# Optimization experiments

Hardware: AMD Instinct MI355X
Metric: run time of the kernel (lower is better)

Reference implementation:

```python
import jax, jax.numpy as jnp
import numpy as np

V, C, T = 4096, 32, 512


def setup_inputs() -> dict:
    key = jax.random.key(0)
    ks = jax.random.split(key, 6)
    return {
        "x": jax.random.normal(ks[0], (V, C, T), dtype=jnp.float32),
        "U_1": jax.random.normal(ks[1], (V,), dtype=jnp.float32),
        "U_2": jax.random.normal(ks[2], (C, V), dtype=jnp.float32),
        "U_3": jax.random.normal(ks[3], (C,), dtype=jnp.float32),
        "b_e": jax.random.normal(ks[4], (C, T, T), dtype=jnp.float32),
        "V_e": jax.random.normal(ks[5], (T, T), dtype=jnp.float32),
    }


def reference(x, U_1, U_2, U_3, b_e, V_e):
    # x: (V, C, T)
    # lhs = (x.permute(2,1,0) @ U_1) @ U_2  -> (T, C) @ (C, V) = (T, V)
    tmp = jnp.einsum("vct,v->tc", x, U_1)          # (T, C)
    lhs = tmp @ U_2                                   # (T, V)
    # rhs = x.permute(2,0,1) @ U_3 -> (T, V)
    rhs = jnp.einsum("vct,c->tv", x, U_3)           # (T, V)
    product = rhs @ lhs.T                             # (T, T)
    # sigmoid(product + b_e) broadcasts to (C, T, T); V_e @ ... -> (C, T, T)
    E = jnp.einsum("ts,csr->ctr", V_e, jax.nn.sigmoid(product + b_e))
    # max-subtract / exp / sum over dim 1 == softmax over axis 1
    return jax.nn.softmax(E, axis=1)
```

## Files before the change

### kernel.cpp

```cpp
#include <hip/hip_runtime.h>

#define V_N 4096
#define C_N 32
#define T_N 512

typedef float f32x4 __attribute__((ext_vector_type(4)));
typedef __bf16 bf16x8 __attribute__((ext_vector_type(8)));

__device__ inline f32x4 fma4(f32x4 a, float b, f32x4 c) {
    f32x4 r;
    r.x = fmaf(a.x, b, c.x); r.y = fmaf(a.y, b, c.y);
    r.z = fmaf(a.z, b, c.z); r.w = fmaf(a.w, b, c.w);
    return r;
}

__global__ __launch_bounds__(256, 1) void k_rt(const float* __restrict__ x,
                                               const float* __restrict__ U1,
                                               const float* __restrict__ U2,
                                               const float* __restrict__ U3,
                                               float* __restrict__ partT,
                                               float* __restrict__ partG) {
    const int vc = blockIdx.x >> 1;
    const int half = blockIdx.x & 1;
    const int tid = threadIdx.x;
    const int w = tid >> 6;
    const int l = tid & 63;
    const int v0 = vc * 16;

    __shared__ f32x4 lsum[2][4][64];

    float u3loc[8];
#pragma unroll
    for (int i = 0; i < 8; ++i) u3loc[i] = U3[w * 8 + i];

    f32x4 accT[8], gacc[8];
#pragma unroll
    for (int i = 0; i < 8; ++i) { accT[i] = (f32x4)0.f; gacc[i] = (f32x4)0.f; }

    const float* xbase = x + (size_t)v0 * (C_N * T_N) + half * 256 + l * 4;

#pragma unroll 1
    for (int vi = 0; vi < 16; ++vi) {
        const float* xp = xbase + (size_t)vi * (C_N * T_N);
        float u1 = U1[v0 + vi];
        int buf = vi & 1;
        f32x4 racc = (f32x4)0.f;
#pragma unroll
        for (int i = 0; i < 8; ++i) {
            f32x4 xv = *(const f32x4*)(xp + (size_t)(w * 8 + i) * T_N);
            accT[i] = fma4(xv, u1, accT[i]);
            racc = fma4(xv, u3loc[i], racc);
        }
        lsum[buf][w][l] = racc;
        __syncthreads();
        f32x4 rhs = (lsum[buf][0][l] + lsum[buf][1][l]) +
                    (lsum[buf][2][l] + lsum[buf][3][l]);
#pragma unroll
        for (int i = 0; i < 8; ++i)
            gacc[i] = fma4(rhs, U2[(size_t)(w * 8 + i) * V_N + v0 + vi], gacc[i]);
    }

    const size_t pbase = (size_t)vc * (C_N * T_N) + half * 256 + l * 4;
#pragma unroll
    for (int i = 0; i < 8; ++i) {
        size_t off = pbase + (size_t)(w * 8 + i) * T_N;
        *(f32x4*)&partT[off] = accT[i];
        *(f32x4*)&partG[off] = gacc[i];
    }
}

__global__ __launch_bounds__(128) void k_redpre(const float* __restrict__ partT,
                                                const float* __restrict__ partG,
                                                float* __restrict__ tmpT,
                                                float* __restrict__ Gc,
                                                const float* __restrict__ Ve,
                                                __bf16* __restrict__ VeHi,
                                                __bf16* __restrict__ VeLo) {
    if (blockIdx.x >= 512) {
        int o = (blockIdx.x - 512) * 128 + threadIdx.x;
        int e = o & 7, lp = (o >> 3) & 63, tile = o >> 9;
        int kk = tile & 15, tt = tile >> 4;
        int t = tt * 16 + (lp & 15);
        int k = kk * 32 + (lp >> 4) * 8 + e;
        float v = Ve[(size_t)t * T_N + k];
        __bf16 h = (__bf16)v;
        VeHi[o] = h;
        VeLo[o] = (__bf16)(v - (float)h);
        return;
    }
    __shared__ f32x4 red[16][8];
    int oid = threadIdx.x & 15;
    int seg = threadIdx.x >> 4;
    int o = blockIdx.x * 16 + oid;
    int isG = o >> 12;
    int oo = o & 4095;
    int c = oo >> 7;
    int tq = oo & 127;
    const float* src = isG ? partG : partT;
    size_t base = (size_t)c * T_N + tq * 4;
    f32x4 s = (f32x4)0.f;
#pragma unroll 4
    for (int vc = seg * 32; vc < seg * 32 + 32; ++vc)
        s += *(const f32x4*)&src[base + (size_t)vc * (C_N * T_N)];
    red[oid][seg] = s;
    __syncthreads();
    if (seg == 0) {
        f32x4 tot = red[oid][0];
#pragma unroll
        for (int k = 1; k < 8; ++k) tot += red[oid][k];
        float* dst = isG ? Gc : tmpT;
        *(f32x4*)&dst[c * T_N + tq * 4] = tot;
    }
}

__global__ __launch_bounds__(256) void k_P2(const float* __restrict__ Gc,
                                            const float* __restrict__ tmpT,
                                            float* __restrict__ P) {
    __shared__ float Gs[32][64];
    __shared__ float Ts[32][64];
    int rbase = blockIdx.x * 64, sbase = blockIdx.y * 64;
    int tid = threadIdx.x;
    int tx = tid & 15, ty = tid >> 4;
    for (int i = tid; i < 2048; i += 256) {
        int cc = i >> 6, j = i & 63;
        Gs[cc][j] = Gc[cc * T_N + sbase + j];
        Ts[cc][j] = tmpT[cc * T_N + rbase + j];
    }
    __syncthreads();
    float acc[4][4] = {};
#pragma unroll
    for (int cc = 0; cc < 32; ++cc) {
        float a[4], b[4];
#pragma unroll
        for (int i = 0; i < 4; ++i) a[i] = Gs[cc][ty * 4 + i];
#pragma unroll
        for (int j = 0; j < 4; ++j) b[j] = Ts[cc][tx * 4 + j];
#pragma unroll
        for (int i = 0; i < 4; ++i)
#pragma unroll
            for (int j = 0; j < 4; ++j) acc[i][j] = fmaf(a[i], b[j], acc[i][j]);
    }
#pragma unroll
    for (int i = 0; i < 4; ++i) {
        f32x4 vv = {acc[i][0], acc[i][1], acc[i][2], acc[i][3]};
        *(f32x4*)&P[(size_t)(sbase + ty * 4 + i) * T_N + rbase + tx * 4] = vv;
    }
}

__global__ __launch_bounds__(512, 4) void k_fused(const float* __restrict__ P,
                                                  const float* __restrict__ be,
                                                  const __bf16* __restrict__ VeHi,
                                                  const __bf16* __restrict__ VeLo,
                                                  float* __restrict__ out) {
    __shared__ __bf16 S[32][512];
    const int rbase = blockIdx.x * 32;
    const int c = blockIdx.y;
    const int tid = threadIdx.x;
    const size_t cTT = (size_t)c * T_N * T_N;

    {
        int r4 = (tid & 7) * 4;
        int s0 = tid >> 3;
        for (int i = 0; i < 8; ++i) {
            int s = i * 64 + s0;
            size_t off = (size_t)s * T_N + rbase + r4;
            f32x4 pv = *(const f32x4*)&P[off];
            f32x4 bv = *(const f32x4*)&be[cTT + off];
#pragma unroll
            for (int j = 0; j < 4; ++j) {
                float vv = pv[j] + bv[j];
                float sg = 1.0f / (1.0f + __expf(-vv));
                int rl = r4 + j;
                S[rl][s ^ ((rl & 7) << 3)] = (__bf16)sg;
            }
        }
    }
    __syncthreads();

    const int lane = tid & 63;
    const int w = tid >> 6;
    const int wt = w & 3;
    const int wr = w >> 2;
    const int lhi = lane >> 4;
    const int llo = lane & 15;

    const bf16x8* fragHi = (const bf16x8*)VeHi;
    const bf16x8* fragLo = (const bf16x8*)VeLo;

    f32x4 acc[8];
#pragma unroll
    for (int mi = 0; mi < 8; ++mi) acc[mi] = (f32x4)0.f;

    for (int k0 = 0; k0 < T_N; k0 += 32) {
        int rr = wr * 16 + llo;
        int g = (k0 >> 3) + lhi;
        bf16x8 b = *(const bf16x8*)&S[rr][(g ^ (rr & 7)) << 3];
#pragma unroll
        for (int mi = 0; mi < 8; ++mi) {
            int tile = (wt * 8 + mi) * 16 + (k0 >> 5);
            bf16x8 ah = fragHi[tile * 64 + lane];
            bf16x8 al = fragLo[tile * 64 + lane];
            acc[mi] = __builtin_amdgcn_mfma_f32_16x16x32_bf16(ah, b, acc[mi], 0, 0, 0);
            acc[mi] = __builtin_amdgcn_mfma_f32_16x16x32_bf16(al, b, acc[mi], 0, 0, 0);
        }
    }
    __syncthreads();

    float* red = (float*)&S[0][0];
    float gmax, gsum;

    {
        float m = -3.4e38f;
#pragma unroll
        for (int mi = 0; mi < 8; ++mi)
#pragma unroll
            for (int q = 0; q < 4; ++q) m = fmaxf(m, acc[mi][q]);
        m = fmaxf(m, __shfl_xor(m, 16));
        m = fmaxf(m, __shfl_xor(m, 32));
        if (lane < 16) red[wt * 32 + wr * 16 + llo] = m;
    }
    __syncthreads();
    {
        int col = wr * 16 + llo;
        gmax = fmaxf(fmaxf(red[col], red[32 + col]),
                     fmaxf(red[64 + col], red[96 + col]));
    }
    {
        float ssum = 0.f;
#pragma unroll
        for (int mi = 0; mi < 8; ++mi)
#pragma unroll
            for (int q = 0; q < 4; ++q) {
                float e = __expf(acc[mi][q] - gmax);
                acc[mi][q] = e;
                ssum += e;
            }
        ssum += __shfl_xor(ssum, 16);
        ssum += __shfl_xor(ssum, 32);
        if (lane < 16) red[128 + wt * 32 + wr * 16 + llo] = ssum;
    }
    __syncthreads();
    {
        int col = wr * 16 + llo;
        gsum = 1.0f / (red[128 + col] + red[128 + 32 + col] +
                       red[128 + 64 + col] + red[128 + 96 + col]);
    }
    {
        int rg = rbase + wr * 16 + llo;
#pragma unroll
        for (int mi = 0; mi < 8; ++mi)
#pragma unroll
            for (int q = 0; q < 4; ++q) {
                int t = wt * 128 + mi * 16 + lhi * 4 + q;
                out[cTT + (size_t)t * T_N + rg] = acc[mi][q] * gsum;
            }
    }
}

extern "C" void kernel_launch(void* const* d_in, const int* in_sizes, int n_in,
                              void* d_out, int out_size, void* d_ws, size_t ws_size,
                              hipStream_t stream) {
    const float* x  = (const float*)d_in[0];
    const float* U1 = (const float*)d_in[1];
    const float* U2 = (const float*)d_in[2];
    const float* U3 = (const float*)d_in[3];
    const float* be = (const float*)d_in[4];
    const float* Ve = (const float*)d_in[5];
    float* out = (float*)d_out;

    float* ws    = (float*)d_ws;
    float* partT = ws;
    float* partG = ws + 4194304;
    float* P     = ws + 8388608;
    __bf16* VeHi = (__bf16*)(ws + 8650752);
    __bf16* VeLo = (__bf16*)(ws + 8781824);
    float* tmpT  = ws + 8912896;
    float* Gc    = ws + 8929280;

    k_rt    <<<512, 256, 0, stream>>>(x, U1, U2, U3, partT, partG);
    k_redpre<<<512 + 2048, 128, 0, stream>>>(partT, partG, tmpT, Gc, Ve, VeHi, VeLo);
    k_P2    <<<dim3(8, 8), 256, 0, stream>>>(Gc, tmpT, P);
    k_fused <<<dim3(16, C_N), 512, 0, stream>>>(P, be, VeHi, VeLo, out);
}
```

Baseline: 119.1 us.

## Double-buffer x loads into LDS via async global_load_lds and vectorize Ve split

The k_rt stream over x now prefetches the next v-slice straight into shared memory with global_load_lds, double-buffered, so global latency overlaps the FMA work. Manual waitcnt and barrier calls replace __syncthreads. U1, U2 and U3 are staged into shared memory once per block instead of being loaded from global memory every iteration. The Ve hi/lo bf16 split is vectorized to four elements per thread, which cuts the preprocessing grid by four times. The risks are wrong vmcnt accounting, since each thread issues eight 16-byte loads per stage, and the larger LDS footprint.

```diff
diff --git a/kernel.cpp b/kernel.cpp
--- a/kernel.cpp
+++ b/kernel.cpp
@@ -5,6 +5,7 @@
 #define T_N 512
 
 typedef float f32x4 __attribute__((ext_vector_type(4)));
+typedef __bf16 bf16x4 __attribute__((ext_vector_type(4)));
 typedef __bf16 bf16x8 __attribute__((ext_vector_type(8)));
 
 __device__ inline f32x4 fma4(f32x4 a, float b, f32x4 c) {
@@ -20,6 +21,12 @@
                                                const float* __restrict__ U3,
                                                float* __restrict__ partT,
                                                float* __restrict__ partG) {
+    __shared__ float xbuf[2][32][256];
+    __shared__ f32x4 lsum[2][4][64];
+    __shared__ float u2s[32][16];
+    __shared__ float u1s[16];
+    __shared__ float u3s[32];
+
     const int vc = blockIdx.x >> 1;
     const int half = blockIdx.x & 1;
     const int tid = threadIdx.x;
@@ -27,11 +34,18 @@
     const int l = tid & 63;
     const int v0 = vc * 16;
 
-    __shared__ f32x4 lsum[2][4][64];
+    if (tid < 16) u1s[tid] = U1[v0 + tid];
+    if (tid < 32) u3s[tid] = U3[tid];
+    {
+        int c = tid >> 3, e = tid & 7;
+        u2s[c][e] = U2[(size_t)c * V_N + v0 + e];
+        u2s[c][e + 8] = U2[(size_t)c * V_N + v0 + e + 8];
+    }
+    __syncthreads();
 
     float u3loc[8];
 #pragma unroll
-    for (int i = 0; i < 8; ++i) u3loc[i] = U3[w * 8 + i];
+    for (int i = 0; i < 8; ++i) u3loc[i] = u3s[w * 8 + i];
 
     f32x4 accT[8], gacc[8];
 #pragma unroll
@@ -39,26 +53,48 @@
 
     const float* xbase = x + (size_t)v0 * (C_N * T_N) + half * 256 + l * 4;
 
+#define STAGE(vi) {                                                          \
+    const float* xp_ = xbase + (size_t)(vi) * (C_N * T_N);                   \
+    _Pragma("unroll")                                                        \
+    for (int i_ = 0; i_ < 8; ++i_) {                                         \
+        __builtin_amdgcn_global_load_lds(                                    \
+            (const __attribute__((address_space(1))) void*)                  \
+                (xp_ + (size_t)(w * 8 + i_) * T_N),                          \
+            (__attribute__((address_space(3))) void*)                        \
+                &xbuf[(vi) & 1][w * 8 + i_][0],                              \
+            16, 0, 0);                                                       \
+    } }
+
+    STAGE(0);
 #pragma unroll 1
     for (int vi = 0; vi < 16; ++vi) {
-        const float* xp = xbase + (size_t)vi * (C_N * T_N);
-        float u1 = U1[v0 + vi];
-        int buf = vi & 1;
+        const int buf = vi & 1;
+        if (vi + 1 < 16) {
+            STAGE(vi + 1);
+            asm volatile("s_waitcnt vmcnt(8)" ::: "memory");
+        } else {
+            asm volatile("s_waitcnt vmcnt(0)" ::: "memory");
+        }
+        __builtin_amdgcn_sched_barrier(0);
+        float u1 = u1s[vi];
         f32x4 racc = (f32x4)0.f;
 #pragma unroll
         for (int i = 0; i < 8; ++i) {
-            f32x4 xv = *(const f32x4*)(xp + (size_t)(w * 8 + i) * T_N);
+            f32x4 xv = *(const f32x4*)&xbuf[buf][w * 8 + i][l * 4];
             accT[i] = fma4(xv, u1, accT[i]);
             racc = fma4(xv, u3loc[i], racc);
         }
         lsum[buf][w][l] = racc;
-        __syncthreads();
+        asm volatile("s_waitcnt lgkmcnt(0)" ::: "memory");
+        __builtin_amdgcn_sched_barrier(0);
+        __builtin_amdgcn_s_barrier();
         f32x4 rhs = (lsum[buf][0][l] + lsum[buf][1][l]) +
                     (lsum[buf][2][l] + lsum[buf][3][l]);
 #pragma unroll
         for (int i = 0; i < 8; ++i)
-            gacc[i] = fma4(rhs, U2[(size_t)(w * 8 + i) * V_N + v0 + vi], gacc[i]);
-    }
+            gacc[i] = fma4(rhs, u2s[w * 8 + i][vi], gacc[i]);
+    }
+#undef STAGE
 
     const size_t pbase = (size_t)vc * (C_N * T_N) + half * 256 + l * 4;
 #pragma unroll
@@ -77,15 +113,20 @@
                                                 __bf16* __restrict__ VeHi,
                                                 __bf16* __restrict__ VeLo) {
     if (blockIdx.x >= 512) {
-        int o = (blockIdx.x - 512) * 128 + threadIdx.x;
-        int e = o & 7, lp = (o >> 3) & 63, tile = o >> 9;
+        int o = ((blockIdx.x - 512) * 128 + threadIdx.x) * 4;
+        int e0 = o & 7, lp = (o >> 3) & 63, tile = o >> 9;
         int kk = tile & 15, tt = tile >> 4;
         int t = tt * 16 + (lp & 15);
-        int k = kk * 32 + (lp >> 4) * 8 + e;
-        float v = Ve[(size_t)t * T_N + k];
-        __bf16 h = (__bf16)v;
-        VeHi[o] = h;
-        VeLo[o] = (__bf16)(v - (float)h);
+        int k = kk * 32 + (lp >> 4) * 8 + e0;
+        f32x4 v = *(const f32x4*)&Ve[(size_t)t * T_N + k];
+        bf16x4 h, lo;
+#pragma unroll
+        for (int j = 0; j < 4; ++j) {
+            h[j] = (__bf16)v[j];
+            lo[j] = (__bf16)(v[j] - (float)h[j]);
+        }
+        *(bf16x4*)&VeHi[o] = h;
+        *(bf16x4*)&VeLo[o] = lo;
         return;
     }
     __shared__ f32x4 red[16][8];
@@ -278,7 +319,7 @@
     float* Gc    = ws + 8929280;
 
     k_rt    <<<512, 256, 0, stream>>>(x, U1, U2, U3, partT, partG);
-    k_redpre<<<512 + 2048, 128, 0, stream>>>(partT, partG, tmpT, Gc, Ve, VeHi, VeLo);
+    k_redpre<<<512 + 512, 128, 0, stream>>>(partT, partG, tmpT, Gc, Ve, VeHi, VeLo);
     k_P2    <<<dim3(8, 8), 256, 0, stream>>>(Gc, tmpT, P);
     k_fused <<<dim3(16, C_N), 512, 0, stream>>>(P, be, VeHi, VeLo, out);
 }
```

After: 116.9 us. About the same (-1.9%).
